# Performance work log

Measured on AMD Instinct MI355X. Metric: run time of the kernel, lower is better.

Reference implementation:

```python
import jax, jax.numpy as jnp
import numpy as np


def _unpack_int4(packed):
    """Unpack bytes (stored as int32 in [0,256)) into signed int4 values in [-8,7].
    packed: [..., K/2] -> [..., K], low nibble first."""
    lo = packed & 0xF
    hi = (packed >> 4) & 0xF
    lo = lo - 16 * (lo >= 8).astype(jnp.int32)
    hi = hi - 16 * (hi >= 8).astype(jnp.int32)
    out = jnp.stack([lo, hi], axis=-1)
    return out.reshape(packed.shape[:-1] + (packed.shape[-1] * 2,))


def setup_inputs() -> dict:
    key = jax.random.key(0)
    ks = jax.random.split(key, 7)
    M, K, N, R = 8192, 4096, 4096, 32
    return {
        "x_quant": jax.random.randint(ks[0], (M, K // 2), 0, 256, dtype=jnp.int32),
        "x_scale": jax.random.uniform(ks[1], (M,), dtype=jnp.float32) * 0.01 + 1e-3,
        "weight": jax.random.randint(ks[2], (N, K // 2), 0, 256, dtype=jnp.int32),
        "weight_scales": jax.random.uniform(ks[3], (N,), dtype=jnp.float32) * 0.01 + 1e-3,
        "bias": jax.random.normal(ks[4], (N,), dtype=jnp.float32) * 0.01,
        "x_r": jax.random.normal(ks[5], (M, R), dtype=jnp.float32),
        "w_outlier": jax.random.normal(ks[6], (N, R), dtype=jnp.float32),
    }


def reference(x_quant, x_scale, weight, weight_scales, bias, x_r, w_outlier):
    # Unpack packed int4 operands: [M,K] and [N,K], values in [-8,7]
    xq = _unpack_int4(x_quant)
    wq = _unpack_int4(weight)
    # Integer GEMM (s4s4 accumulate in int32), then fused dequant + bias
    acc = jnp.matmul(xq, wq.T)  # [M, N] int32
    out = acc.astype(jnp.float32) * x_scale[:, None] * weight_scales[None, :] + bias[None, :]
    # Low-rank outlier correction: addmm_(x_r, w_outlier.T)
    out = out + jnp.matmul(x_r, w_outlier.T)
    return out
```

## Files before the change

### kernel.cpp

```cpp
#include <hip/hip_runtime.h>

#define M_ 8192
#define K_ 4096
#define N_ 4096
#define R_ 32
#define KP_ (K_ / 2)

#define BM 128
#define BN 128
#define BK 128

typedef __attribute__((ext_vector_type(4))) int    i32x4;
typedef __attribute__((ext_vector_type(4))) float  f32x4;
typedef __attribute__((ext_vector_type(8))) __bf16 bf16x8;

__device__ __forceinline__ void gload16(const void* g, void* l) {
  __builtin_amdgcn_global_load_lds(
      (const __attribute__((address_space(1))) unsigned int*)g,
      (__attribute__((address_space(3))) unsigned int*)l, 16, 0, 0);
}

__device__ __forceinline__ unsigned nib2(int b) {
  unsigned lo = (unsigned)(((b & 15) ^ 8) - 8) & 0xFFu;
  unsigned hi = (unsigned)((((b >> 4) & 15) ^ 8) - 8) & 0xFFu;
  return lo | (hi << 8);
}

__global__ void repack_int4(const int* __restrict__ in, unsigned* __restrict__ out, int n4) {
  int stride = gridDim.x * blockDim.x;
  for (int i = blockIdx.x * blockDim.x + threadIdx.x; i < n4; i += stride) {
    int4 v = ((const int4*)in)[i];
    uint2 o;
    o.x = nib2(v.x) | (nib2(v.y) << 16);
    o.y = nib2(v.z) | (nib2(v.w) << 16);
    ((uint2*)out)[i] = o;
  }
}

__device__ __forceinline__ unsigned short f2b(float x) {
  unsigned u = __float_as_uint(x);
  return (unsigned short)((u + 0x7FFFu + ((u >> 16) & 1u)) >> 16);
}

__global__ void f2bf4(const float* __restrict__ in, unsigned short* __restrict__ out, int n4) {
  int stride = gridDim.x * blockDim.x;
  for (int i = blockIdx.x * blockDim.x + threadIdx.x; i < n4; i += stride) {
    float4 f = ((const float4*)in)[i];
    ushort4 o;
    o.x = f2b(f.x); o.y = f2b(f.y); o.z = f2b(f.z); o.w = f2b(f.w);
    ((ushort4*)out)[i] = o;
  }
}

__global__ __launch_bounds__(256, 3) void gemm_w4a4(
    const signed char* __restrict__ x8, const signed char* __restrict__ w8,
    const unsigned short* __restrict__ xrb, const unsigned short* __restrict__ wob,
    const float* __restrict__ xscale, const float* __restrict__ wscale,
    const float* __restrict__ bias, float* __restrict__ out)
{
  __shared__ __align__(16) signed char lds[2 * BM * BK];
  signed char* As = lds;
  signed char* Bs = lds + BM * BK;

  const int t    = threadIdx.x;
  const int w    = t >> 6;
  const int lrow = t & 15;
  const int lgrp = (t >> 4) & 3;
  const int wr   = w >> 1, wc = w & 1;
  const int m0   = (blockIdx.x & 63) * BM;
  const int n0   = (blockIdx.x >> 6) * BN;

  i32x4 acc[4][4] = {};

  for (int kt = 0; kt < K_ / BK; ++kt) {
    __syncthreads();
    const size_t kb = (size_t)kt * BK;
    #pragma unroll
    for (int i = 0; i < 4; ++i) {
      int idx  = i * 4096 + t * 16;
      int row  = idx >> 7;
      int gcol = (((idx >> 4) & 7) ^ (row & 7)) << 4;
      gload16(x8 + (size_t)(m0 + row) * K_ + kb + gcol, As + i * 4096 + (w << 10));
      gload16(w8 + (size_t)(n0 + row) * K_ + kb + gcol, Bs + i * 4096 + (w << 10));
    }
    __syncthreads();
    #pragma unroll
    for (int ks = 0; ks < 2; ++ks) {
      i32x4 af[4], bf[4];
      #pragma unroll
      for (int f = 0; f < 4; ++f) {
        int ra = wr * 64 + f * 16 + lrow;
        af[f] = *(const i32x4*)(As + ra * BK + ((((ks << 2) + lgrp) ^ (ra & 7)) << 4));
        int rb = wc * 64 + f * 16 + lrow;
        bf[f] = *(const i32x4*)(Bs + rb * BK + ((((ks << 2) + lgrp) ^ (rb & 7)) << 4));
      }
      #pragma unroll
      for (int fm = 0; fm < 4; ++fm)
        #pragma unroll
        for (int fn = 0; fn < 4; ++fn)
          acc[fm][fn] = __builtin_amdgcn_mfma_i32_16x16x64_i8(af[fm], bf[fn], acc[fm][fn], 0, 0, 0);
    }
  }

  float swv[4], bv[4];
  #pragma unroll
  for (int fn = 0; fn < 4; ++fn) {
    int cg = n0 + wc * 64 + fn * 16 + lrow;
    swv[fn] = wscale[cg];
    bv[fn]  = bias[cg];
  }
  float sxv[4][4];
  #pragma unroll
  for (int fm = 0; fm < 4; ++fm)
    #pragma unroll
    for (int j = 0; j < 4; ++j)
      sxv[fm][j] = xscale[m0 + wr * 64 + fm * 16 + lgrp * 4 + j];

  __syncthreads();
  #pragma unroll
  for (int i = 0; i < 2; ++i) {
    int idx = i * 4096 + t * 16;
    int row = idx >> 6, col = idx & 63;
    gload16((const char*)xrb + (size_t)(m0 + row) * 64 + col, lds + i * 4096 + (w << 10));
    gload16((const char*)wob + (size_t)(n0 + row) * 64 + col, lds + 8192 + i * 4096 + (w << 10));
  }
  __syncthreads();

  const unsigned short* xr_s = (const unsigned short*)lds;
  const unsigned short* wo_s = (const unsigned short*)(lds + 8192);
  bf16x8 ar[4], br[4];
  #pragma unroll
  for (int f = 0; f < 4; ++f) {
    ar[f] = *(const bf16x8*)(xr_s + (wr * 64 + f * 16 + lrow) * 32 + lgrp * 8);
    br[f] = *(const bf16x8*)(wo_s + (wc * 64 + f * 16 + lrow) * 32 + lgrp * 8);
  }
  #pragma unroll
  for (int fm = 0; fm < 4; ++fm) {
    #pragma unroll
    for (int fn = 0; fn < 4; ++fn) {
      f32x4 z = {0.0f, 0.0f, 0.0f, 0.0f};
      f32x4 c = __builtin_amdgcn_mfma_f32_16x16x32_bf16(ar[fm], br[fn], z, 0, 0, 0);
      #pragma unroll
      for (int j = 0; j < 4; ++j) {
        int rg = m0 + wr * 64 + fm * 16 + lgrp * 4 + j;
        int cg = n0 + wc * 64 + fn * 16 + lrow;
        out[(size_t)rg * N_ + cg] =
            (float)acc[fm][fn][j] * sxv[fm][j] * swv[fn] + c[j] + bv[fn];
      }
    }
  }
}

extern "C" void kernel_launch(void* const* d_in, const int* in_sizes, int n_in,
                              void* d_out, int out_size, void* d_ws, size_t ws_size,
                              hipStream_t stream) {
  const int*   x_quant   = (const int*)d_in[0];
  const float* x_scale   = (const float*)d_in[1];
  const int*   weight    = (const int*)d_in[2];
  const float* w_scales  = (const float*)d_in[3];
  const float* bias      = (const float*)d_in[4];
  const float* x_r       = (const float*)d_in[5];
  const float* w_outlier = (const float*)d_in[6];
  float* out = (float*)d_out;

  char* ws = (char*)d_ws;
  signed char*    x8  = (signed char*)ws;
  signed char*    w8  = (signed char*)(ws + (size_t)M_ * K_);
  unsigned short* xrb = (unsigned short*)(ws + (size_t)M_ * K_ + (size_t)N_ * K_);
  unsigned short* wob = xrb + (size_t)M_ * R_;

  repack_int4<<<2048, 256, 0, stream>>>(x_quant, (unsigned*)x8, M_ * KP_ / 4);
  repack_int4<<<2048, 256, 0, stream>>>(weight,  (unsigned*)w8, N_ * KP_ / 4);
  f2bf4<<<256, 256, 0, stream>>>(x_r, xrb, M_ * R_ / 4);
  f2bf4<<<128, 256, 0, stream>>>(w_outlier, wob, N_ * R_ / 4);

  gemm_w4a4<<<(M_ / BM) * (N_ / BN), 256, 0, stream>>>(
      x8, w8, xrb, wob, x_scale, w_scales, bias, out);
}
```

Baseline: 160.4 us.

## Use 256x256 tiles with 4-stage async LDS pipeline and 8 waves

Enlarges the block tile to 256x256 with BK=64 and 512 threads. It stages global-to-LDS loads three tiles ahead in a 4-buffer ring, using explicit vmcnt waits and split barriers with setprio around the MFMA bursts. LDS is laid out in MFMA fragment order, which removes the swizzle. The grid is reordered for L2 locality, and the low-rank operands are read straight from global memory. The goal is to hide memory latency and raise arithmetic intensity of the int8 MFMA GEMM. In exchange it uses 128KB of dynamic LDS, more accumulator registers per thread, and has tricky hand-tuned wait counts.

Result: slower. 183.0 us (+14.1%).

```diff
diff --git a/kernel.cpp b/kernel.cpp
--- a/kernel.cpp
+++ b/kernel.cpp
@@ -6,9 +6,14 @@
 #define R_ 32
 #define KP_ (K_ / 2)
 
-#define BM 128
-#define BN 128
-#define BK 128
+#define BM 256
+#define BN 256
+#define BK 64
+#define NT (K_ / BK)
+#define NBUF 4
+#define ABUF_SZ 16384
+#define TILE_SZ 32768
+#define GRID ((M_ / BM) * (N_ / BN))
 
 typedef __attribute__((ext_vector_type(4))) int    i32x4;
 typedef __attribute__((ext_vector_type(4))) float  f32x4;
@@ -52,100 +57,134 @@
   }
 }
 
-__global__ __launch_bounds__(256, 3) void gemm_w4a4(
+__global__ __launch_bounds__(512, 2) void gemm_w4a4(
     const signed char* __restrict__ x8, const signed char* __restrict__ w8,
     const unsigned short* __restrict__ xrb, const unsigned short* __restrict__ wob,
     const float* __restrict__ xscale, const float* __restrict__ wscale,
     const float* __restrict__ bias, float* __restrict__ out)
 {
-  __shared__ __align__(16) signed char lds[2 * BM * BK];
-  signed char* As = lds;
-  signed char* Bs = lds + BM * BK;
+  extern __shared__ __align__(16) char lds[];
 
   const int t    = threadIdx.x;
   const int w    = t >> 6;
-  const int lrow = t & 15;
-  const int lgrp = (t >> 4) & 3;
-  const int wr   = w >> 1, wc = w & 1;
-  const int m0   = (blockIdx.x & 63) * BM;
-  const int n0   = (blockIdx.x >> 6) * BN;
-
-  i32x4 acc[4][4] = {};
-
-  for (int kt = 0; kt < K_ / BK; ++kt) {
-    __syncthreads();
-    const size_t kb = (size_t)kt * BK;
-    #pragma unroll
-    for (int i = 0; i < 4; ++i) {
-      int idx  = i * 4096 + t * 16;
-      int row  = idx >> 7;
-      int gcol = (((idx >> 4) & 7) ^ (row & 7)) << 4;
-      gload16(x8 + (size_t)(m0 + row) * K_ + kb + gcol, As + i * 4096 + (w << 10));
-      gload16(w8 + (size_t)(n0 + row) * K_ + kb + gcol, Bs + i * 4096 + (w << 10));
+  const int l    = t & 63;
+  const int lrow = l & 15;
+  const int lgrp = l >> 4;
+  const int wr   = w >> 2;
+  const int wc   = w & 3;
+
+  const int swz  = (blockIdx.x & 7) * (GRID / 8) + (blockIdx.x >> 3);
+  const int m0   = (swz & 31) * BM;
+  const int n0   = (swz >> 5) * BN;
+
+  const signed char* aS0 = x8 + (size_t)(m0 + w * 16 + lrow) * K_ + lgrp * 16;
+  const signed char* aS1 = x8 + (size_t)(m0 + (8 + w) * 16 + lrow) * K_ + lgrp * 16;
+  const signed char* bS0 = w8 + (size_t)(n0 + w * 16 + lrow) * K_ + lgrp * 16;
+  const signed char* bS1 = w8 + (size_t)(n0 + (8 + w) * 16 + lrow) * K_ + lgrp * 16;
+
+#define STAGE_A(tile)                                                        \
+  { char* d = lds + ((tile) & 3) * TILE_SZ + w * 1024;                       \
+    gload16(aS0 + (size_t)(tile) * BK, d);                                   \
+    gload16(aS1 + (size_t)(tile) * BK, d + 8192); }
+#define STAGE_B(tile)                                                        \
+  { char* d = lds + ((tile) & 3) * TILE_SZ + ABUF_SZ + w * 1024;             \
+    gload16(bS0 + (size_t)(tile) * BK, d);                                   \
+    gload16(bS1 + (size_t)(tile) * BK, d + 8192); }
+#define FENCE asm volatile("" ::: "memory")
+
+  i32x4 acc[8][4] = {};
+
+  STAGE_A(0) STAGE_B(0)
+  STAGE_A(1) STAGE_B(1)
+  STAGE_A(2) STAGE_B(2)
+  asm volatile("s_waitcnt vmcnt(8)" ::: "memory");
+  __builtin_amdgcn_s_barrier();
+  FENCE;
+
+  for (int kt = 0; kt < NT; ++kt) {
+    const char* Ab = lds + (kt & 3) * TILE_SZ;
+    const char* Bb = Ab + ABUF_SZ;
+
+    i32x4 bf[4], af0[4];
+    #pragma unroll
+    for (int n = 0; n < 4; ++n)
+      bf[n] = *(const i32x4*)(Bb + (wc * 4 + n) * 1024 + l * 16);
+    #pragma unroll
+    for (int m = 0; m < 4; ++m)
+      af0[m] = *(const i32x4*)(Ab + (wr * 8 + m) * 1024 + l * 16);
+    if (kt < NT - 3) STAGE_A(kt + 3)
+    FENCE;
+    __builtin_amdgcn_s_barrier();
+    FENCE;
+    __builtin_amdgcn_s_setprio(1);
+    #pragma unroll
+    for (int m = 0; m < 4; ++m)
+      #pragma unroll
+      for (int n = 0; n < 4; ++n)
+        acc[m][n] = __builtin_amdgcn_mfma_i32_16x16x64_i8(af0[m], bf[n], acc[m][n], 0, 0, 0);
+    __builtin_amdgcn_s_setprio(0);
+    FENCE;
+    __builtin_amdgcn_s_barrier();
+    FENCE;
+
+    i32x4 af1[4];
+    #pragma unroll
+    for (int m = 0; m < 4; ++m)
+      af1[m] = *(const i32x4*)(Ab + (wr * 8 + 4 + m) * 1024 + l * 16);
+    if (kt < NT - 3) {
+      STAGE_B(kt + 3)
+      asm volatile("s_waitcnt vmcnt(8)" ::: "memory");
+    } else if (kt == NT - 3) {
+      asm volatile("s_waitcnt vmcnt(4)" ::: "memory");
+    } else if (kt == NT - 2) {
+      asm volatile("s_waitcnt vmcnt(0)" ::: "memory");
     }
-    __syncthreads();
-    #pragma unroll
-    for (int ks = 0; ks < 2; ++ks) {
-      i32x4 af[4], bf[4];
+    FENCE;
+    __builtin_amdgcn_s_barrier();
+    FENCE;
+    __builtin_amdgcn_s_setprio(1);
+    #pragma unroll
+    for (int m = 0; m < 4; ++m)
       #pragma unroll
-      for (int f = 0; f < 4; ++f) {
-        int ra = wr * 64 + f * 16 + lrow;
-        af[f] = *(const i32x4*)(As + ra * BK + ((((ks << 2) + lgrp) ^ (ra & 7)) << 4));
-        int rb = wc * 64 + f * 16 + lrow;
-        bf[f] = *(const i32x4*)(Bs + rb * BK + ((((ks << 2) + lgrp) ^ (rb & 7)) << 4));
-      }
-      #pragma unroll
-      for (int fm = 0; fm < 4; ++fm)
-        #pragma unroll
-        for (int fn = 0; fn < 4; ++fn)
-          acc[fm][fn] = __builtin_amdgcn_mfma_i32_16x16x64_i8(af[fm], bf[fn], acc[fm][fn], 0, 0, 0);
-    }
-  }
-
+      for (int n = 0; n < 4; ++n)
+        acc[4 + m][n] = __builtin_amdgcn_mfma_i32_16x16x64_i8(af1[m], bf[n], acc[4 + m][n], 0, 0, 0);
+    __builtin_amdgcn_s_setprio(0);
+    FENCE;
+    __builtin_amdgcn_s_barrier();
+    FENCE;
+  }
+
+  f32x4 sxv[8];
+  #pragma unroll
+  for (int m = 0; m < 8; ++m)
+    sxv[m] = *(const f32x4*)(xscale + m0 + wr * 128 + m * 16 + lgrp * 4);
   float swv[4], bv[4];
   #pragma unroll
-  for (int fn = 0; fn < 4; ++fn) {
-    int cg = n0 + wc * 64 + fn * 16 + lrow;
-    swv[fn] = wscale[cg];
-    bv[fn]  = bias[cg];
-  }
-  float sxv[4][4];
-  #pragma unroll
-  for (int fm = 0; fm < 4; ++fm)
-    #pragma unroll
-    for (int j = 0; j < 4; ++j)
-      sxv[fm][j] = xscale[m0 + wr * 64 + fm * 16 + lgrp * 4 + j];
-
-  __syncthreads();
-  #pragma unroll
-  for (int i = 0; i < 2; ++i) {
-    int idx = i * 4096 + t * 16;
-    int row = idx >> 6, col = idx & 63;
-    gload16((const char*)xrb + (size_t)(m0 + row) * 64 + col, lds + i * 4096 + (w << 10));
-    gload16((const char*)wob + (size_t)(n0 + row) * 64 + col, lds + 8192 + i * 4096 + (w << 10));
-  }
-  __syncthreads();
-
-  const unsigned short* xr_s = (const unsigned short*)lds;
-  const unsigned short* wo_s = (const unsigned short*)(lds + 8192);
-  bf16x8 ar[4], br[4];
-  #pragma unroll
-  for (int f = 0; f < 4; ++f) {
-    ar[f] = *(const bf16x8*)(xr_s + (wr * 64 + f * 16 + lrow) * 32 + lgrp * 8);
-    br[f] = *(const bf16x8*)(wo_s + (wc * 64 + f * 16 + lrow) * 32 + lgrp * 8);
-  }
-  #pragma unroll
-  for (int fm = 0; fm < 4; ++fm) {
-    #pragma unroll
-    for (int fn = 0; fn < 4; ++fn) {
+  for (int n = 0; n < 4; ++n) {
+    int cg = n0 + wc * 64 + n * 16 + lrow;
+    swv[n] = wscale[cg];
+    bv[n]  = bias[cg];
+  }
+  bf16x8 ar[8], br[4];
+  #pragma unroll
+  for (int m = 0; m < 8; ++m)
+    ar[m] = *(const bf16x8*)(xrb + (size_t)(m0 + wr * 128 + m * 16 + lrow) * R_ + lgrp * 8);
+  #pragma unroll
+  for (int n = 0; n < 4; ++n)
+    br[n] = *(const bf16x8*)(wob + (size_t)(n0 + wc * 64 + n * 16 + lrow) * R_ + lgrp * 8);
+
+  #pragma unroll
+  for (int m = 0; m < 8; ++m) {
+    #pragma unroll
+    for (int n = 0; n < 4; ++n) {
       f32x4 z = {0.0f, 0.0f, 0.0f, 0.0f};
-      f32x4 c = __builtin_amdgcn_mfma_f32_16x16x32_bf16(ar[fm], br[fn], z, 0, 0, 0);
+      f32x4 c = __builtin_amdgcn_mfma_f32_16x16x32_bf16(ar[m], br[n], z, 0, 0, 0);
       #pragma unroll
       for (int j = 0; j < 4; ++j) {
-        int rg = m0 + wr * 64 + fm * 16 + lgrp * 4 + j;
-        int cg = n0 + wc * 64 + fn * 16 + lrow;
+        int rg = m0 + wr * 128 + m * 16 + lgrp * 4 + j;
+        int cg = n0 + wc * 64 + n * 16 + lrow;
         out[(size_t)rg * N_ + cg] =
-            (float)acc[fm][fn][j] * sxv[fm][j] * swv[fn] + c[j] + bv[fn];
+            (float)acc[m][n][j] * sxv[m][j] * swv[n] + c[j] + bv[n];
       }
     }
   }
@@ -169,11 +208,15 @@
   unsigned short* xrb = (unsigned short*)(ws + (size_t)M_ * K_ + (size_t)N_ * K_);
   unsigned short* wob = xrb + (size_t)M_ * R_;
 
+  (void)hipFuncSetAttribute((const void*)gemm_w4a4,
+                            hipFuncAttributeMaxDynamicSharedMemorySize,
+                            NBUF * TILE_SZ);
+
   repack_int4<<<2048, 256, 0, stream>>>(x_quant, (unsigned*)x8, M_ * KP_ / 4);
   repack_int4<<<2048, 256, 0, stream>>>(weight,  (unsigned*)w8, N_ * KP_ / 4);
   f2bf4<<<256, 256, 0, stream>>>(x_r, xrb, M_ * R_ / 4);
   f2bf4<<<128, 256, 0, stream>>>(w_outlier, wob, N_ * R_ / 4);
 
-  gemm_w4a4<<<(M_ / BM) * (N_ / BN), 256, 0, stream>>>(
+  gemm_w4a4<<<GRID, 512, NBUF * TILE_SZ, stream>>>(
       x8, w8, xrb, wob, x_scale, w_scales, bias, out);
 }
```
